# Kernel tuning notes

Hardware: AMD Instinct MI355X
Metric: run time of the kernel (lower is better)

The kernel has to match this reference:

```python
import jax, jax.numpy as jnp
import numpy as np

B, L, M, C = 32, 688, 4, 32  # batch, otsl_sequence_length (= layout_prompt_length), max targets per box, tag vocab


def setup_inputs() -> dict:
    key = jax.random.key(0)
    ks = jax.random.split(key, 8)
    tag_logits = jax.random.normal(ks[0], (B, L, C), jnp.float32)
    pointer_logits = jax.random.normal(ks[1], (B, L, L), jnp.float32)
    empty_pointer_logits = jax.random.normal(ks[2], (B, 1, L), jnp.float32)
    tag_targets = jax.random.randint(ks[3], (B, L), 0, C)
    box = jax.random.randint(ks[4], (B, L, M), 0, L)
    keep = jax.random.bernoulli(ks[5], 0.5, (B, L, M))
    box_indices = jnp.where(keep, box, -1)  # -1 = padded / invalid target
    data_tag_mask = jax.random.bernoulli(ks[6], 0.3, (B, 2 * L))
    attention_mask = jax.random.bernoulli(ks[7], 0.8, (B, 2 * L)) | data_tag_mask
    return {
        'tag_logits': tag_logits,
        'pointer_logits': pointer_logits,
        'empty_pointer_logits': empty_pointer_logits,
        'tag_targets': tag_targets,
        'box_indices': box_indices,
        'data_tag_mask': data_tag_mask,
        'attention_mask': attention_mask,
    }


def reference(tag_logits, pointer_logits, empty_pointer_logits,
              tag_targets, box_indices, data_tag_mask, attention_mask):
    Bq, Lq, Cq = tag_logits.shape

    # ---- tag (cls) loss: mean cross-entropy over B*S positions ----
    logp = jax.nn.log_softmax(tag_logits, axis=-1)
    cls_loss = -jnp.mean(jnp.take_along_axis(logp, tag_targets[..., None], axis=-1))

    # ---- pointer loss: masked softmax over sequence positions ----
    seq_mask = data_tag_mask[:, Lq:]                                  # (B, L)
    mx = jnp.max(pointer_logits, axis=-1, keepdims=True)              # unmasked max, as in torch code
    exp_l = jnp.exp(pointer_logits - mx)                              # (B, L, L)
    denom = jnp.sum(exp_l * seq_mask[:, None, :], axis=-1, keepdims=True) + 1e-10
    # scatter target_mask[b, i, box_indices[b, i, m]] = True for valid entries
    valid = box_indices != -1                                         # (B, L, M)
    tgt = jnp.clip(box_indices, 0, Lq - 1)
    b_ix = jnp.arange(Bq)[:, None, None]
    r_ix = jnp.arange(Lq)[None, :, None]
    target_mask = jnp.zeros((Bq, Lq, Lq), bool).at[b_ix, r_ix, tgt].max(valid)
    losses = -jnp.log(exp_l / denom + 1e-10)                          # (B, L, L)
    masked = losses * (target_mask & seq_mask[:, None, :])
    cnt = jnp.sum(masked != 0)
    ptr_loss = jnp.where(cnt == 0, 0.0, jnp.sum(masked) / jnp.maximum(cnt, 1))

    # ---- empty pointer loss: BCE-with-logits, mean over attended positions ----
    seq2 = attention_mask[:, Lq:]                                     # (B, L)
    data2 = data_tag_mask[:, Lq:]
    targets = (seq2 & ~data2).astype(jnp.float32)
    x = empty_pointer_logits[:, 0, :]                                 # (B, L)
    bce = jnp.maximum(x, 0.0) - x * targets + jnp.log1p(jnp.exp(-jnp.abs(x)))
    vm = seq2.astype(jnp.float32)
    empty_ptr_loss = jnp.sum(bce * vm) / jnp.maximum(jnp.sum(vm), 1.0)

    # forward() returns early: total = cls + ptr + empty (no lambdas, contrastive dead code)
    total = cls_loss + ptr_loss + empty_ptr_loss
    return total, cls_loss, ptr_loss, empty_ptr_loss
```

## Files before the change

### kernel.cpp

```cpp
#include <hip/hip_runtime.h>
#include <hip/hip_bf16.h>
#include <math.h>

#define BB 32
#define LL 688
#define MM 4
#define CC 32
#define ROWS (BB * LL)
#define WPB 4
#define NBLK (ROWS / WPB)

struct Partial { float4 a; float4 b; };

__global__ __launch_bounds__(256) void fused_kernel(
    const float* __restrict__ tag_logits,
    const float* __restrict__ pl,
    const float* __restrict__ epl,
    const int* __restrict__ tag_targets,
    const int* __restrict__ box,
    const int* __restrict__ dtm,
    const int* __restrict__ am,
    Partial* __restrict__ partials)
{
    __shared__ float red[WPB][5];
    const int wave = threadIdx.x >> 6;
    const int lane = threadIdx.x & 63;
    const int row  = blockIdx.x * WPB + wave;
    const int b    = row / LL;
    const int j    = row - b * LL;

    const float4* rowp  = (const float4*)(pl + (size_t)row * LL);
    const int*    mrow  = dtm + b * (2 * LL) + LL;
    const int4*   maskp = (const int4*)mrow;

    const float4 v0 = rowp[lane];
    const float4 v1 = rowp[lane + 64];
    const bool has2 = (lane < 172 - 128);
    const float4 v2 = has2 ? rowp[lane + 128]
                           : make_float4(-INFINITY, -INFINITY, -INFINITY, -INFINITY);

    float mx = fmaxf(fmaxf(fmaxf(v0.x, v0.y), fmaxf(v0.z, v0.w)),
                     fmaxf(fmaxf(v1.x, v1.y), fmaxf(v1.z, v1.w)));
    mx = fmaxf(mx, fmaxf(fmaxf(v2.x, v2.y), fmaxf(v2.z, v2.w)));
    #pragma unroll
    for (int off = 32; off >= 1; off >>= 1)
        mx = fmaxf(mx, __shfl_xor(mx, off));

    const int4 m0 = maskp[lane];
    const int4 m1 = maskp[lane + 64];
    const int4 m2 = has2 ? maskp[lane + 128] : make_int4(0, 0, 0, 0);
    float s = 0.f;
    if (m0.x) s += expf(v0.x - mx);
    if (m0.y) s += expf(v0.y - mx);
    if (m0.z) s += expf(v0.z - mx);
    if (m0.w) s += expf(v0.w - mx);
    if (m1.x) s += expf(v1.x - mx);
    if (m1.y) s += expf(v1.y - mx);
    if (m1.z) s += expf(v1.z - mx);
    if (m1.w) s += expf(v1.w - mx);
    if (m2.x) s += expf(v2.x - mx);
    if (m2.y) s += expf(v2.y - mx);
    if (m2.z) s += expf(v2.z - mx);
    if (m2.w) s += expf(v2.w - mx);
    #pragma unroll
    for (int off = 32; off >= 1; off >>= 1)
        s += __shfl_xor(s, off);

    float x = tag_logits[(size_t)row * CC + (lane & 31)];
    float cm = x;
    #pragma unroll
    for (int off = 16; off >= 1; off >>= 1)
        cm = fmaxf(cm, __shfl_xor(cm, off, 32));
    float cs = expf(x - cm);
    #pragma unroll
    for (int off = 16; off >= 1; off >>= 1)
        cs += __shfl_xor(cs, off, 32);
    const int tgt = tag_targets[row];
    const float xt = __shfl(x, tgt, 32);

    if (lane == 0) {
        const float denom = s + 1e-10f;
        const int* bx = box + (size_t)row * MM;
        int t0 = -1, t1 = -1, t2 = -1;
        float lsum = 0.f;
        int lcnt = 0;
        #pragma unroll
        for (int mi = 0; mi < MM; ++mi) {
            int t = bx[mi];
            if (t < 0) continue;
            if (t > LL - 1) t = LL - 1;
            if (t == t0 || t == t1 || t == t2) continue;
            if (t0 < 0) t0 = t; else if (t1 < 0) t1 = t; else t2 = t;
            if (!mrow[t]) continue;
            const float xj = pl[(size_t)row * LL + t];
            const float p = expf(xj - mx) / denom + 1e-10f;
            const float v = -logf(p);
            lsum += v;
            if (v != 0.0f) lcnt++;
        }
        const int off2  = b * (2 * LL) + LL + j;
        const int seq2  = am[off2];
        const int data2 = dtm[off2];
        const float xe  = epl[row];
        const float te  = (seq2 && !data2) ? 1.f : 0.f;
        const float bce = fmaxf(xe, 0.f) - xe * te + log1pf(expf(-fabsf(xe)));

        red[wave][0] = (cm + logf(cs)) - xt;
        red[wave][1] = lsum;
        red[wave][2] = (float)lcnt;
        red[wave][3] = seq2 ? bce : 0.f;
        red[wave][4] = seq2 ? 1.f : 0.f;
    }
    __syncthreads();
    if (threadIdx.x == 0) {
        Partial p;
        p.a.x = red[0][0] + red[1][0] + red[2][0] + red[3][0];
        p.a.y = red[0][1] + red[1][1] + red[2][1] + red[3][1];
        p.a.z = red[0][2] + red[1][2] + red[2][2] + red[3][2];
        p.a.w = red[0][3] + red[1][3] + red[2][3] + red[3][3];
        p.b = make_float4(red[0][4] + red[1][4] + red[2][4] + red[3][4], 0.f, 0.f, 0.f);
        partials[blockIdx.x] = p;
    }
}

__global__ __launch_bounds__(1024) void reduce_kernel(const Partial* __restrict__ partials,
                                                      float* __restrict__ out)
{
    __shared__ float sm[16][5];
    float cls = 0.f, ptr = 0.f, cnt = 0.f, bce = 0.f, vm = 0.f;
    for (int i = threadIdx.x; i < NBLK; i += 1024) {
        const Partial p = partials[i];
        cls += p.a.x; ptr += p.a.y; cnt += p.a.z; bce += p.a.w; vm += p.b.x;
    }
    #pragma unroll
    for (int off = 32; off >= 1; off >>= 1) {
        cls += __shfl_xor(cls, off);
        ptr += __shfl_xor(ptr, off);
        cnt += __shfl_xor(cnt, off);
        bce += __shfl_xor(bce, off);
        vm  += __shfl_xor(vm,  off);
    }
    const int wv = threadIdx.x >> 6;
    if ((threadIdx.x & 63) == 0) {
        sm[wv][0] = cls; sm[wv][1] = ptr; sm[wv][2] = cnt;
        sm[wv][3] = bce; sm[wv][4] = vm;
    }
    __syncthreads();
    if (threadIdx.x == 0) {
        float tc = 0.f, tp = 0.f, tn = 0.f, tb = 0.f, tv = 0.f;
        #pragma unroll
        for (int i = 0; i < 16; ++i) {
            tc += sm[i][0]; tp += sm[i][1]; tn += sm[i][2];
            tb += sm[i][3]; tv += sm[i][4];
        }
        const float cls_loss = tc / (float)ROWS;
        const float ptr_loss = (tn == 0.f) ? 0.f : tp / fmaxf(tn, 1.f);
        const float emp_loss = tb / fmaxf(tv, 1.f);
        out[0] = cls_loss + ptr_loss + emp_loss;
        out[1] = cls_loss;
        out[2] = ptr_loss;
        out[3] = emp_loss;
    }
}

extern "C" void kernel_launch(void* const* d_in, const int* in_sizes, int n_in,
                              void* d_out, int out_size, void* d_ws, size_t ws_size,
                              hipStream_t stream) {
    const float* tag_logits           = (const float*)d_in[0];
    const float* pointer_logits       = (const float*)d_in[1];
    const float* empty_pointer_logits = (const float*)d_in[2];
    const int*   tag_targets          = (const int*)d_in[3];
    const int*   box_indices          = (const int*)d_in[4];
    const int*   data_tag_mask        = (const int*)d_in[5];
    const int*   attention_mask       = (const int*)d_in[6];
    float* out = (float*)d_out;
    Partial* partials = (Partial*)d_ws;

    fused_kernel<<<NBLK, 256, 0, stream>>>(tag_logits, pointer_logits,
                                           empty_pointer_logits, tag_targets,
                                           box_indices, data_tag_mask,
                                           attention_mask, partials);
    reduce_kernel<<<1, 1024, 0, stream>>>(partials, out);
}
```

Measured before the change: 118.9 us.

## Process four rows per wave with shared mask and lane-parallel tail work

Each wave now handles four pointer rows instead of one. The data_tag_mask row is loaded and converted to floats once and reused across the four rows, and the masked exponent sum becomes branchless FMAs using fast __expf. The per-row target, cls and BCE work that a single lane did serially is spread across lanes with shuffles. The block count drops by four and the final reduce runs with 256 threads. This costs more registers per thread, and the fast math intrinsics may shift results slightly.

Result: faster. 108.5 us (-8.8%).

```diff
diff --git a/kernel.cpp b/kernel.cpp
--- a/kernel.cpp
+++ b/kernel.cpp
@@ -7,10 +7,36 @@
 #define MM 4
 #define CC 32
 #define ROWS (BB * LL)
+#define RPW 4
 #define WPB 4
-#define NBLK (ROWS / WPB)
+#define RPB (RPW * WPB)
+#define NBLK (ROWS / RPB)
 
 struct Partial { float4 a; float4 b; };
+
+__device__ __forceinline__ float max12(float4 x, float4 y, float4 z) {
+    return fmaxf(fmaxf(fmaxf(fmaxf(x.x, x.y), fmaxf(x.z, x.w)),
+                       fmaxf(fmaxf(y.x, y.y), fmaxf(y.z, y.w))),
+                 fmaxf(fmaxf(z.x, z.y), fmaxf(z.z, z.w)));
+}
+
+__device__ __forceinline__ float msum12(float4 x, float4 y, float4 z,
+                                        float4 f0, float4 f1, float4 f2, float m) {
+    float s = 0.f;
+    s = fmaf(f0.x, __expf(x.x - m), s);
+    s = fmaf(f0.y, __expf(x.y - m), s);
+    s = fmaf(f0.z, __expf(x.z - m), s);
+    s = fmaf(f0.w, __expf(x.w - m), s);
+    s = fmaf(f1.x, __expf(y.x - m), s);
+    s = fmaf(f1.y, __expf(y.y - m), s);
+    s = fmaf(f1.z, __expf(y.z - m), s);
+    s = fmaf(f1.w, __expf(y.w - m), s);
+    s = fmaf(f2.x, __expf(z.x - m), s);
+    s = fmaf(f2.y, __expf(z.y - m), s);
+    s = fmaf(f2.z, __expf(z.z - m), s);
+    s = fmaf(f2.w, __expf(z.w - m), s);
+    return s;
+}
 
 __global__ __launch_bounds__(256) void fused_kernel(
     const float* __restrict__ tag_logits,
@@ -25,91 +51,127 @@
     __shared__ float red[WPB][5];
     const int wave = threadIdx.x >> 6;
     const int lane = threadIdx.x & 63;
-    const int row  = blockIdx.x * WPB + wave;
-    const int b    = row / LL;
-    const int j    = row - b * LL;
-
-    const float4* rowp  = (const float4*)(pl + (size_t)row * LL);
-    const int*    mrow  = dtm + b * (2 * LL) + LL;
-    const int4*   maskp = (const int4*)mrow;
-
-    const float4 v0 = rowp[lane];
-    const float4 v1 = rowp[lane + 64];
-    const bool has2 = (lane < 172 - 128);
-    const float4 v2 = has2 ? rowp[lane + 128]
-                           : make_float4(-INFINITY, -INFINITY, -INFINITY, -INFINITY);
-
-    float mx = fmaxf(fmaxf(fmaxf(v0.x, v0.y), fmaxf(v0.z, v0.w)),
-                     fmaxf(fmaxf(v1.x, v1.y), fmaxf(v1.z, v1.w)));
-    mx = fmaxf(mx, fmaxf(fmaxf(v2.x, v2.y), fmaxf(v2.z, v2.w)));
-    #pragma unroll
-    for (int off = 32; off >= 1; off >>= 1)
-        mx = fmaxf(mx, __shfl_xor(mx, off));
-
-    const int4 m0 = maskp[lane];
-    const int4 m1 = maskp[lane + 64];
-    const int4 m2 = has2 ? maskp[lane + 128] : make_int4(0, 0, 0, 0);
-    float s = 0.f;
-    if (m0.x) s += expf(v0.x - mx);
-    if (m0.y) s += expf(v0.y - mx);
-    if (m0.z) s += expf(v0.z - mx);
-    if (m0.w) s += expf(v0.w - mx);
-    if (m1.x) s += expf(v1.x - mx);
-    if (m1.y) s += expf(v1.y - mx);
-    if (m1.z) s += expf(v1.z - mx);
-    if (m1.w) s += expf(v1.w - mx);
-    if (m2.x) s += expf(v2.x - mx);
-    if (m2.y) s += expf(v2.y - mx);
-    if (m2.z) s += expf(v2.z - mx);
-    if (m2.w) s += expf(v2.w - mx);
-    #pragma unroll
-    for (int off = 32; off >= 1; off >>= 1)
-        s += __shfl_xor(s, off);
-
-    float x = tag_logits[(size_t)row * CC + (lane & 31)];
-    float cm = x;
-    #pragma unroll
-    for (int off = 16; off >= 1; off >>= 1)
-        cm = fmaxf(cm, __shfl_xor(cm, off, 32));
-    float cs = expf(x - cm);
-    #pragma unroll
-    for (int off = 16; off >= 1; off >>= 1)
-        cs += __shfl_xor(cs, off, 32);
-    const int tgt = tag_targets[row];
-    const float xt = __shfl(x, tgt, 32);
+    const int row0 = blockIdx.x * RPB + wave * RPW;
+    const int bat  = row0 / LL;
+    const int jcol0 = row0 - bat * LL;
+
+    const int* mrow = dtm + bat * (2 * LL) + LL;
+    const int4* maskp = (const int4*)mrow;
+    const bool has2 = (lane < 44);
+
+    const int4 mi0 = maskp[lane];
+    const int4 mi1 = maskp[lane + 64];
+    const int4 mi2 = has2 ? maskp[lane + 128] : make_int4(0, 0, 0, 0);
+    const float4 f0 = make_float4(mi0.x ? 1.f : 0.f, mi0.y ? 1.f : 0.f,
+                                  mi0.z ? 1.f : 0.f, mi0.w ? 1.f : 0.f);
+    const float4 f1 = make_float4(mi1.x ? 1.f : 0.f, mi1.y ? 1.f : 0.f,
+                                  mi1.z ? 1.f : 0.f, mi1.w ? 1.f : 0.f);
+    const float4 f2 = make_float4(mi2.x ? 1.f : 0.f, mi2.y ? 1.f : 0.f,
+                                  mi2.z ? 1.f : 0.f, mi2.w ? 1.f : 0.f);
+
+    const float4 NEGV = make_float4(-INFINITY, -INFINITY, -INFINITY, -INFINITY);
+    const float4* rp0 = (const float4*)(pl + (size_t)(row0 + 0) * LL);
+    const float4* rp1 = (const float4*)(pl + (size_t)(row0 + 1) * LL);
+    const float4* rp2 = (const float4*)(pl + (size_t)(row0 + 2) * LL);
+    const float4* rp3 = (const float4*)(pl + (size_t)(row0 + 3) * LL);
+
+    const float4 a0 = rp0[lane], a1 = rp0[lane + 64], a2 = has2 ? rp0[lane + 128] : NEGV;
+    const float4 c0 = rp1[lane], c1 = rp1[lane + 64], c2 = has2 ? rp1[lane + 128] : NEGV;
+    const float4 d0 = rp2[lane], d1 = rp2[lane + 64], d2 = has2 ? rp2[lane + 128] : NEGV;
+    const float4 e0 = rp3[lane], e1 = rp3[lane + 64], e2 = has2 ? rp3[lane + 128] : NEGV;
+
+    float pm0 = max12(a0, a1, a2);
+    float pm1 = max12(c0, c1, c2);
+    float pm2 = max12(d0, d1, d2);
+    float pm3 = max12(e0, e1, e2);
+    #pragma unroll
+    for (int off = 32; off >= 1; off >>= 1) {
+        pm0 = fmaxf(pm0, __shfl_xor(pm0, off));
+        pm1 = fmaxf(pm1, __shfl_xor(pm1, off));
+        pm2 = fmaxf(pm2, __shfl_xor(pm2, off));
+        pm3 = fmaxf(pm3, __shfl_xor(pm3, off));
+    }
+
+    float ps0 = msum12(a0, a1, a2, f0, f1, f2, pm0);
+    float ps1 = msum12(c0, c1, c2, f0, f1, f2, pm1);
+    float ps2 = msum12(d0, d1, d2, f0, f1, f2, pm2);
+    float ps3 = msum12(e0, e1, e2, f0, f1, f2, pm3);
+    #pragma unroll
+    for (int off = 32; off >= 1; off >>= 1) {
+        ps0 += __shfl_xor(ps0, off);
+        ps1 += __shfl_xor(ps1, off);
+        ps2 += __shfl_xor(ps2, off);
+        ps3 += __shfl_xor(ps3, off);
+    }
+
+    const int rl  = lane & 15;
+    const int r   = rl >> 2;
+    const int mi  = rl & 3;
+    const int rowr = row0 + r;
+    const float mxr = (r == 0) ? pm0 : (r == 1) ? pm1 : (r == 2) ? pm2 : pm3;
+    const float dnr = ((r == 0) ? ps0 : (r == 1) ? ps1 : (r == 2) ? ps2 : ps3) + 1e-10f;
+
+    const int t = box[(size_t)rowr * MM + mi];
+    const int ta  = __shfl(t, (lane & ~3));
+    const int tb  = __shfl(t, (lane & ~3) + 1);
+    const int tc2 = __shfl(t, (lane & ~3) + 2);
+    const bool dup = (mi > 0 && t == ta) || (mi > 1 && t == tb) || (mi > 2 && t == tc2);
+    const bool valid = (t >= 0);
+    const int tcl = t < 0 ? 0 : (t > LL - 1 ? LL - 1 : t);
+
+    float contrib = 0.f, ccnt = 0.f;
+    if (valid && !dup && mrow[tcl]) {
+        const float xj = pl[(size_t)rowr * LL + tcl];
+        const float p = __expf(xj - mxr) / dnr + 1e-10f;
+        const float v = -__logf(p);
+        contrib = v;
+        ccnt = (v != 0.0f) ? 1.f : 0.f;
+    }
+    contrib += __shfl_xor(contrib, 1); contrib += __shfl_xor(contrib, 2);
+    ccnt    += __shfl_xor(ccnt, 1);    ccnt    += __shfl_xor(ccnt, 2);
+    const float ptr_sum = __shfl(contrib, 0) + __shfl(contrib, 4) +
+                          __shfl(contrib, 8) + __shfl(contrib, 12);
+    const float ptr_cnt = __shfl(ccnt, 0) + __shfl(ccnt, 4) +
+                          __shfl(ccnt, 8) + __shfl(ccnt, 12);
+
+    float cls_tot = 0.f;
+    #pragma unroll
+    for (int pass = 0; pass < 2; ++pass) {
+        const int rowc = row0 + pass * 2 + (lane >> 5);
+        const float x = tag_logits[(size_t)rowc * CC + (lane & 31)];
+        float cm = x;
+        #pragma unroll
+        for (int off = 16; off >= 1; off >>= 1)
+            cm = fmaxf(cm, __shfl_xor(cm, off, 32));
+        float cs = __expf(x - cm);
+        #pragma unroll
+        for (int off = 16; off >= 1; off >>= 1)
+            cs += __shfl_xor(cs, off, 32);
+        const int tg = tag_targets[rowc];
+        const float xt = __shfl(x, tg + (lane & 32));
+        const float c = (cm + __logf(cs)) - xt;
+        cls_tot += __shfl(c, 0) + __shfl(c, 32);
+    }
+
+    const int rb = lane & 3;
+    const int rowb = row0 + rb;
+    const int offb = bat * (2 * LL) + LL + (jcol0 + rb);
+    const int seq2  = am[offb];
+    const int data2 = dtm[offb];
+    const float xe = epl[rowb];
+    const float te = (seq2 && !data2) ? 1.f : 0.f;
+    const float bce = fmaxf(xe, 0.f) - xe * te + log1pf(__expf(-fabsf(xe)));
+    float bsum = seq2 ? bce : 0.f;
+    float vsum = seq2 ? 1.f : 0.f;
+    bsum += __shfl_xor(bsum, 1); bsum += __shfl_xor(bsum, 2);
+    vsum += __shfl_xor(vsum, 1); vsum += __shfl_xor(vsum, 2);
 
     if (lane == 0) {
-        const float denom = s + 1e-10f;
-        const int* bx = box + (size_t)row * MM;
-        int t0 = -1, t1 = -1, t2 = -1;
-        float lsum = 0.f;
-        int lcnt = 0;
-        #pragma unroll
-        for (int mi = 0; mi < MM; ++mi) {
-            int t = bx[mi];
-            if (t < 0) continue;
-            if (t > LL - 1) t = LL - 1;
-            if (t == t0 || t == t1 || t == t2) continue;
-            if (t0 < 0) t0 = t; else if (t1 < 0) t1 = t; else t2 = t;
-            if (!mrow[t]) continue;
-            const float xj = pl[(size_t)row * LL + t];
-            const float p = expf(xj - mx) / denom + 1e-10f;
-            const float v = -logf(p);
-            lsum += v;
-            if (v != 0.0f) lcnt++;
-        }
-        const int off2  = b * (2 * LL) + LL + j;
-        const int seq2  = am[off2];
-        const int data2 = dtm[off2];
-        const float xe  = epl[row];
-        const float te  = (seq2 && !data2) ? 1.f : 0.f;
-        const float bce = fmaxf(xe, 0.f) - xe * te + log1pf(expf(-fabsf(xe)));
-
-        red[wave][0] = (cm + logf(cs)) - xt;
-        red[wave][1] = lsum;
-        red[wave][2] = (float)lcnt;
-        red[wave][3] = seq2 ? bce : 0.f;
-        red[wave][4] = seq2 ? 1.f : 0.f;
+        red[wave][0] = cls_tot;
+        red[wave][1] = ptr_sum;
+        red[wave][2] = ptr_cnt;
+        red[wave][3] = bsum;
+        red[wave][4] = vsum;
     }
     __syncthreads();
     if (threadIdx.x == 0) {
@@ -123,33 +185,32 @@
     }
 }
 
-__global__ __launch_bounds__(1024) void reduce_kernel(const Partial* __restrict__ partials,
-                                                      float* __restrict__ out)
+__global__ __launch_bounds__(256) void reduce_kernel(const Partial* __restrict__ partials,
+                                                     float* __restrict__ out)
 {
-    __shared__ float sm[16][5];
-    float cls = 0.f, ptr = 0.f, cnt = 0.f, bce = 0.f, vm = 0.f;
-    for (int i = threadIdx.x; i < NBLK; i += 1024) {
-        const Partial p = partials[i];
-        cls += p.a.x; ptr += p.a.y; cnt += p.a.z; bce += p.a.w; vm += p.b.x;
+    __shared__ float sm[4][5];
+    float c = 0.f, p = 0.f, n = 0.f, e = 0.f, v = 0.f;
+    for (int i = threadIdx.x; i < NBLK; i += 256) {
+        const Partial q = partials[i];
+        c += q.a.x; p += q.a.y; n += q.a.z; e += q.a.w; v += q.b.x;
     }
     #pragma unroll
     for (int off = 32; off >= 1; off >>= 1) {
-        cls += __shfl_xor(cls, off);
-        ptr += __shfl_xor(ptr, off);
-        cnt += __shfl_xor(cnt, off);
-        bce += __shfl_xor(bce, off);
-        vm  += __shfl_xor(vm,  off);
+        c += __shfl_xor(c, off);
+        p += __shfl_xor(p, off);
+        n += __shfl_xor(n, off);
+        e += __shfl_xor(e, off);
+        v += __shfl_xor(v, off);
     }
     const int wv = threadIdx.x >> 6;
     if ((threadIdx.x & 63) == 0) {
-        sm[wv][0] = cls; sm[wv][1] = ptr; sm[wv][2] = cnt;
-        sm[wv][3] = bce; sm[wv][4] = vm;
+        sm[wv][0] = c; sm[wv][1] = p; sm[wv][2] = n; sm[wv][3] = e; sm[wv][4] = v;
     }
     __syncthreads();
     if (threadIdx.x == 0) {
         float tc = 0.f, tp = 0.f, tn = 0.f, tb = 0.f, tv = 0.f;
         #pragma unroll
-        for (int i = 0; i < 16; ++i) {
+        for (int i = 0; i < 4; ++i) {
             tc += sm[i][0]; tp += sm[i][1]; tn += sm[i][2];
             tb += sm[i][3]; tv += sm[i][4];
         }
@@ -180,5 +241,5 @@
                                            empty_pointer_logits, tag_targets,
                                            box_indices, data_tag_mask,
                                            attention_mask, partials);
-    reduce_kernel<<<1, 1024, 0, stream>>>(partials, out);
-}
+    reduce_kernel<<<1, 256, 0, stream>>>(partials, out);
+}
```
